# Kernel tuning notes

Hardware: AMD Instinct MI355X
Metric: run time of the kernel (lower is better)

The kernel has to match this reference:

```python
import jax, jax.numpy as jnp
import numpy as np

N = 100000
E = 3200000
IN_DIM, HID_DIM, OUT_DIM = 29, 64, 2


def setup_inputs() -> dict:
    key = jax.random.key(0)
    k1, k2, k3, k4, k5 = jax.random.split(key, 5)
    x = jax.random.normal(k1, (N, IN_DIM), dtype=jnp.float32)
    edge_index = jax.random.randint(k2, (2, E), 0, N, dtype=jnp.int64)
    # GCNConv params: glorot-ish weights, zero bias (bias added after aggregation)
    W1 = jax.random.normal(k3, (IN_DIM, HID_DIM), dtype=jnp.float32) * (1.0 / np.sqrt(IN_DIM))
    b1 = jnp.zeros((HID_DIM,), dtype=jnp.float32)
    W2 = jax.random.normal(k4, (HID_DIM, OUT_DIM), dtype=jnp.float32) * (1.0 / np.sqrt(HID_DIM))
    b2 = jnp.zeros((OUT_DIM,), dtype=jnp.float32)
    return {"x": x, "edge_index": edge_index, "W1": W1, "b1": b1, "W2": W2, "b2": b2}


def _gcn_norm(edge_index, n_nodes):
    # PyG gcn_norm with add_self_loops=True, symmetric D^-1/2 A D^-1/2
    loop = jnp.arange(n_nodes, dtype=edge_index.dtype)
    src = jnp.concatenate([edge_index[0], loop])
    dst = jnp.concatenate([edge_index[1], loop])
    deg = jax.ops.segment_sum(jnp.ones_like(dst, dtype=jnp.float32), dst, num_segments=n_nodes)
    dinv = jnp.where(deg > 0, jax.lax.rsqrt(deg), 0.0)
    norm = dinv[src] * dinv[dst]  # [E + N]
    return src, dst, norm


def _gcn_conv(x, src, dst, norm, W, b):
    h = x @ W                      # [N, d_out] -- transform first (smaller msgs)
    msg = h[src] * norm[:, None]   # [E+N, d_out] gather + scale
    out = jax.ops.segment_sum(msg, dst, num_segments=x.shape[0])  # scatter-add
    return out + b


def reference(x, edge_index, W1, b1, W2, b2):
    src, dst, norm = _gcn_norm(edge_index, x.shape[0])
    h = _gcn_conv(x, src, dst, norm, W1, b1)
    h = jax.nn.relu(h)
    out = _gcn_conv(h, src, dst, norm, W2, b2)
    return out
```

## Files before the change

kernel.cpp:

```cpp
#include <hip/hip_runtime.h>

#define N_NODES 100000
#define N_EDGES 3200000
#define IN_DIM  29
#define HID_DIM 64
#define NBUCK   1563
#define BNODES  64
#define CAP     2560
#define EPT     32
#define EPB     16384

#define OFF_CUR   0
#define OFF_DEGC  2048
#define OFF_DINV  102080
#define OFF_ROWS  202112
#define OFF_ROWE  302144
#define OFF_ZS    402176
#define OFF_EBUF  602240
#define OFF_XS    4603520

typedef unsigned uv2 __attribute__((ext_vector_type(2)));

static __device__ __forceinline__ unsigned short f2bf(float f) {
    unsigned u = __float_as_uint(f);
    u += 0x7fffu + ((u >> 16) & 1u);
    return (unsigned short)(u >> 16);
}

static __device__ __forceinline__ void unpack_add(float4& acc, uv2 a) {
    acc.x += __uint_as_float(a.x << 16);
    acc.y += __uint_as_float(a.x & 0xFFFF0000u);
    acc.z += __uint_as_float(a.y << 16);
    acc.w += __uint_as_float(a.y & 0xFFFF0000u);
}

__global__ __launch_bounds__(512) void partition_kernel(const int* __restrict__ ei,
        int* __restrict__ gcursor, int* __restrict__ ebuf) {
    __shared__ int lhist[NBUCK];
    __shared__ int lcur[NBUCK];
    int tid = threadIdx.x;
    for (int i = tid; i < NBUCK; i += 512) lhist[i] = 0;
    __syncthreads();

    int base = blockIdx.x * EPB + tid * EPT;
    int dv[EPT], sv[EPT];
    bool valid = (base < N_EDGES);
    if (valid) {
        const int4* dp = (const int4*)(ei + N_EDGES + base);
        const int4* sp = (const int4*)(ei + base);
        #pragma unroll
        for (int q = 0; q < 8; ++q) {
            int4 t = dp[q];
            dv[4*q+0] = t.x; dv[4*q+1] = t.y; dv[4*q+2] = t.z; dv[4*q+3] = t.w;
            int4 u = sp[q];
            sv[4*q+0] = u.x; sv[4*q+1] = u.y; sv[4*q+2] = u.z; sv[4*q+3] = u.w;
        }
        #pragma unroll
        for (int j = 0; j < EPT; ++j) atomicAdd(&lhist[dv[j] >> 6], 1);
    }
    __syncthreads();
    for (int i = tid; i < NBUCK; i += 512) {
        int c = lhist[i];
        lcur[i] = c ? (atomicAdd(&gcursor[i], c) + i * CAP) : 0;
    }
    __syncthreads();
    if (valid) {
        #pragma unroll
        for (int j = 0; j < EPT; ++j) {
            int d = dv[j];
            int pos = atomicAdd(&lcur[d >> 6], 1);
            ebuf[pos] = sv[j] | ((d & 63) << 17);
        }
    }
}

__global__ __launch_bounds__(256) void degcnt_kernel(const int* __restrict__ gcursor,
        const int* __restrict__ ebuf, const float* __restrict__ x,
        int* __restrict__ degc, float* __restrict__ dinv,
        unsigned int* __restrict__ xsb) {
    __shared__ int   cnt[BNODES];
    __shared__ float dls[BNODES];
    int b = blockIdx.x, tid = threadIdx.x;
    if (tid < BNODES) cnt[tid] = 0;
    __syncthreads();
    int base = b * CAP, sz = gcursor[b];
    for (int j = tid; j < sz; j += 256)
        atomicAdd(&cnt[((unsigned)ebuf[base + j]) >> 17], 1);
    __syncthreads();
    if (tid < BNODES) {
        int node = b * BNODES + tid;
        if (node < N_NODES) {
            int c = cnt[tid];
            degc[node] = c;
            float dn = rsqrtf((float)c + 1.0f);
            dinv[node] = dn;
            dls[tid] = dn;
        }
    }
    __syncthreads();
    for (int i = tid; i < BNODES * 16; i += 256) {
        int dl = i >> 4, kp = i & 15;
        int nd = b * BNODES + dl;
        if (nd < N_NODES) {
            float dn = dls[dl];
            int k0 = kp * 2, k1 = k0 + 1;
            float f0 = (k0 < IN_DIM) ? x[nd * IN_DIM + k0] * dn : 0.0f;
            float f1 = (k1 < IN_DIM) ? x[nd * IN_DIM + k1] * dn : 0.0f;
            xsb[(size_t)nd * 16 + kp] = (unsigned)f2bf(f0) | ((unsigned)f2bf(f1) << 16);
        }
    }
}

__global__ __launch_bounds__(256) void sortfused_kernel(const unsigned int* __restrict__ xs_,
        const int* __restrict__ gcursor, int* __restrict__ ebuf,
        const int* __restrict__ degc,
        int* __restrict__ rowStart, int* __restrict__ rowEnd,
        const float* __restrict__ W1, const float* __restrict__ b1,
        const float* __restrict__ W2, float* __restrict__ zs) {
    __shared__ float w1s[IN_DIM * HID_DIM];
    __shared__ float b1s[HID_DIM];
    __shared__ float w2s[HID_DIM * 2];
    __shared__ int   cnt[BNODES];
    __shared__ int   rs_l[BNODES];
    __shared__ int   cur[BNODES];
    __shared__ int   stage[CAP];
    int tid = threadIdx.x, b = blockIdx.x;
    for (int i = tid; i < IN_DIM * HID_DIM; i += 256) w1s[i] = W1[i];
    if (tid < HID_DIM) {
        b1s[tid] = b1[tid];
        w2s[tid * 2 + 0] = W2[tid * 2 + 0];
        w2s[tid * 2 + 1] = W2[tid * 2 + 1];
    }
    int base = b * CAP, sz = gcursor[b];
    if (tid < BNODES) {
        int node = b * BNODES + tid;
        cnt[tid] = (node < N_NODES) ? degc[node] : 0;
    }
    __syncthreads();

    if (tid < 64) {
        int c = cnt[tid];
        int incl = c;
        #pragma unroll
        for (int off = 1; off < 64; off <<= 1) {
            int t = __shfl_up(incl, off);
            if (tid >= off) incl += t;
        }
        int excl = incl - c;
        rs_l[tid] = excl;
        cur[tid]  = excl;
        int node = b * BNODES + tid;
        if (node < N_NODES) {
            rowStart[node] = base + excl;
            rowEnd[node]   = base + excl + c;
        }
    }
    __syncthreads();

    for (int j = tid; j < sz; j += 256) {
        unsigned p = (unsigned)ebuf[base + j];
        int pos = atomicAdd(&cur[p >> 17], 1);
        stage[pos] = p & 0x1FFFF;
    }
    __syncthreads();
    for (int j = tid; j < sz; j += 256)
        ebuf[base + j] = stage[j];

    int wave = tid >> 6, lane = tid & 63;
    int q = lane >> 3, m = lane & 7;
    const uv2* xsbv = (const uv2*)xs_;
    for (int dl = wave; dl < BNODES; dl += 4) {
        int node = b * BNODES + dl;
        if (node >= N_NODES) break;
        float4 acc = make_float4(0.f, 0.f, 0.f, 0.f);
        if (q == 0)
            unpack_add(acc, xsbv[(size_t)node * 8 + m]);
        int rs = rs_l[dl], re = rs + cnt[dl];
        int last = re - 1;
        for (int j = rs + q; j < re; j += 32) {
            int j1 = j + 8, j2 = j + 16, j3 = j + 24;
            int s0 = stage[j];
            int s1 = stage[min(j1, last)];
            int s2 = stage[min(j2, last)];
            int s3 = stage[min(j3, last)];
            uv2 a0 = xsbv[(size_t)s0 * 8 + m];
            uv2 a1 = xsbv[(size_t)s1 * 8 + m];
            uv2 a2 = xsbv[(size_t)s2 * 8 + m];
            uv2 a3 = xsbv[(size_t)s3 * 8 + m];
            unpack_add(acc, a0);
            if (j1 < re) unpack_add(acc, a1);
            if (j2 < re) unpack_add(acc, a2);
            if (j3 < re) unpack_add(acc, a3);
        }
        #pragma unroll
        for (int msk = 8; msk <= 32; msk <<= 1) {
            acc.x += __shfl_xor(acc.x, msk);
            acc.y += __shfl_xor(acc.y, msk);
            acc.z += __shfl_xor(acc.z, msk);
            acc.w += __shfl_xor(acc.w, msk);
        }
        float dn = rsqrtf((float)cnt[dl] + 1.0f);
        acc.x *= dn; acc.y *= dn; acc.z *= dn; acc.w *= dn;

        float h = b1s[lane];
        #pragma unroll
        for (int kk = 0; kk < IN_DIM; ++kk) {
            float comp = ((kk & 3) == 0) ? acc.x : ((kk & 3) == 1) ? acc.y
                       : ((kk & 3) == 2) ? acc.z : acc.w;
            h = fmaf(__shfl(comp, kk >> 2), w1s[kk * HID_DIM + lane], h);
        }
        h = fmaxf(h, 0.0f);

        float z0 = h * w2s[lane * 2 + 0];
        float z1 = h * w2s[lane * 2 + 1];
        #pragma unroll
        for (int off = 32; off > 0; off >>= 1) {
            z0 += __shfl_down(z0, off);
            z1 += __shfl_down(z1, off);
        }
        if (lane == 0) {
            zs[node * 2 + 0] = z0 * dn;
            zs[node * 2 + 1] = z1 * dn;
        }
    }
}

__global__ __launch_bounds__(256) void agg2_kernel(const float* __restrict__ zs,
        const int* __restrict__ rowStart, const int* __restrict__ rowEnd,
        const int* __restrict__ ebuf, const float* __restrict__ dinv,
        const float* __restrict__ b2, float* __restrict__ out) {
    int tid = threadIdx.x;
    int node = blockIdx.x * 16 + (tid >> 4);
    if (node >= N_NODES) return;
    int gl = tid & 15;
    const float2* zs2 = (const float2*)zs;
    float a0 = 0.0f, a1 = 0.0f, c0 = 0.0f, c1 = 0.0f;
    int rs = rowStart[node], re = rowEnd[node];
    int last = re - 1;
    for (int j = rs + gl; j < re; j += 32) {
        int j1 = j + 16;
        float2 za = zs2[ebuf[j]];
        float2 zb = zs2[ebuf[min(j1, last)]];
        a0 += za.x; a1 += za.y;
        if (j1 < re) { c0 += zb.x; c1 += zb.y; }
    }
    a0 += c0; a1 += c1;
    a0 += __shfl_xor(a0, 8); a1 += __shfl_xor(a1, 8);
    a0 += __shfl_xor(a0, 4); a1 += __shfl_xor(a1, 4);
    a0 += __shfl_xor(a0, 2); a1 += __shfl_xor(a1, 2);
    a0 += __shfl_xor(a0, 1); a1 += __shfl_xor(a1, 1);
    if (gl == 0) {
        float dn = dinv[node];
        float2 zself = zs2[node];
        float2 o;
        o.x = dn * (a0 + zself.x) + b2[0];
        o.y = dn * (a1 + zself.y) + b2[1];
        ((float2*)out)[node] = o;
    }
}

extern "C" void kernel_launch(void* const* d_in, const int* in_sizes, int n_in,
                              void* d_out, int out_size, void* d_ws, size_t ws_size,
                              hipStream_t stream) {
    const float* x  = (const float*)d_in[0];
    const int*   ei = (const int*)d_in[1];
    const float* W1 = (const float*)d_in[2];
    const float* b1 = (const float*)d_in[3];
    const float* W2 = (const float*)d_in[4];
    const float* b2 = (const float*)d_in[5];
    float* out = (float*)d_out;

    int*   wsi      = (int*)d_ws;
    float* wsf      = (float*)d_ws;
    int*   gcursor  = wsi + OFF_CUR;
    int*   degc     = wsi + OFF_DEGC;
    float* dinv     = wsf + OFF_DINV;
    int*   rowStart = wsi + OFF_ROWS;
    int*   rowEnd   = wsi + OFF_ROWE;
    float* zs       = wsf + OFF_ZS;
    int*   ebuf     = wsi + OFF_EBUF;
    unsigned int* xsb = (unsigned int*)(wsi + OFF_XS);

    hipMemsetAsync(gcursor, 0, NBUCK * sizeof(int), stream);
    partition_kernel<<<(N_EDGES + EPB - 1) / EPB, 512, 0, stream>>>(ei, gcursor, ebuf);
    degcnt_kernel<<<NBUCK, 256, 0, stream>>>(gcursor, ebuf, x, degc, dinv, xsb);
    sortfused_kernel<<<NBUCK, 256, 0, stream>>>(xsb, gcursor, ebuf, degc,
                                                rowStart, rowEnd, W1, b1, W2, zs);
    agg2_kernel<<<(N_NODES + 15) / 16, 256, 0, stream>>>(zs, rowStart, rowEnd, ebuf, dinv, b2, out);
}
```

Measured before the change: 237.9 us.

## Use coarser 256-node buckets with sub-block filtering and drop CSR writeback

Edges are now partitioned into 391 buckets of 256 destination nodes instead of 1563 buckets of 64. Each bucket is handled by 8 sub-blocks that each scan the whole bucket and keep only the edges for their own 32 nodes. This removes the sorted-ebuf writeback and the rowStart/rowEnd arrays. The second aggregation now accumulates into shared memory with atomics over the bucket, instead of walking per-node CSR rows. The cost is that every bucket is read 8 times in both the sort/fuse and aggregation kernels, and shared-memory float atomics replace register reductions.

```diff
diff --git a/kernel.cpp b/kernel.cpp
--- a/kernel.cpp
+++ b/kernel.cpp
@@ -4,20 +4,21 @@
 #define N_EDGES 3200000
 #define IN_DIM  29
 #define HID_DIM 64
-#define NBUCK   1563
-#define BNODES  64
-#define CAP     2560
-#define EPT     32
-#define EPB     16384
+#define NBUCK   391
+#define CNODES  256
+#define CAP     10240
+#define SUB     8
+#define SNODES  32
+#define CAP_S   1408
+#define EPT     8
+#define EPB     4096
 
 #define OFF_CUR   0
-#define OFF_DEGC  2048
-#define OFF_DINV  102080
-#define OFF_ROWS  202112
-#define OFF_ROWE  302144
-#define OFF_ZS    402176
-#define OFF_EBUF  602240
-#define OFF_XS    4603520
+#define OFF_DEGC  512
+#define OFF_DINV  100512
+#define OFF_ZS    200512
+#define OFF_EBUF  400512
+#define OFF_XS    4404352
 
 typedef unsigned uv2 __attribute__((ext_vector_type(2)));
 
@@ -49,14 +50,14 @@
         const int4* dp = (const int4*)(ei + N_EDGES + base);
         const int4* sp = (const int4*)(ei + base);
         #pragma unroll
-        for (int q = 0; q < 8; ++q) {
-            int4 t = dp[q];
-            dv[4*q+0] = t.x; dv[4*q+1] = t.y; dv[4*q+2] = t.z; dv[4*q+3] = t.w;
-            int4 u = sp[q];
-            sv[4*q+0] = u.x; sv[4*q+1] = u.y; sv[4*q+2] = u.z; sv[4*q+3] = u.w;
-        }
-        #pragma unroll
-        for (int j = 0; j < EPT; ++j) atomicAdd(&lhist[dv[j] >> 6], 1);
+        for (int qq = 0; qq < 2; ++qq) {
+            int4 t = dp[qq];
+            dv[4*qq+0] = t.x; dv[4*qq+1] = t.y; dv[4*qq+2] = t.z; dv[4*qq+3] = t.w;
+            int4 u = sp[qq];
+            sv[4*qq+0] = u.x; sv[4*qq+1] = u.y; sv[4*qq+2] = u.z; sv[4*qq+3] = u.w;
+        }
+        #pragma unroll
+        for (int j = 0; j < EPT; ++j) atomicAdd(&lhist[dv[j] >> 8], 1);
     }
     __syncthreads();
     for (int i = tid; i < NBUCK; i += 512) {
@@ -68,27 +69,27 @@
         #pragma unroll
         for (int j = 0; j < EPT; ++j) {
             int d = dv[j];
-            int pos = atomicAdd(&lcur[d >> 6], 1);
-            ebuf[pos] = sv[j] | ((d & 63) << 17);
-        }
-    }
-}
-
-__global__ __launch_bounds__(256) void degcnt_kernel(const int* __restrict__ gcursor,
+            int pos = atomicAdd(&lcur[d >> 8], 1);
+            ebuf[pos] = sv[j] | ((d & 255) << 17);
+        }
+    }
+}
+
+__global__ __launch_bounds__(1024) void degcnt_kernel(const int* __restrict__ gcursor,
         const int* __restrict__ ebuf, const float* __restrict__ x,
         int* __restrict__ degc, float* __restrict__ dinv,
         unsigned int* __restrict__ xsb) {
-    __shared__ int   cnt[BNODES];
-    __shared__ float dls[BNODES];
+    __shared__ int   cnt[CNODES];
+    __shared__ float dls[CNODES];
     int b = blockIdx.x, tid = threadIdx.x;
-    if (tid < BNODES) cnt[tid] = 0;
+    if (tid < CNODES) cnt[tid] = 0;
     __syncthreads();
     int base = b * CAP, sz = gcursor[b];
-    for (int j = tid; j < sz; j += 256)
+    for (int j = tid; j < sz; j += 1024)
         atomicAdd(&cnt[((unsigned)ebuf[base + j]) >> 17], 1);
     __syncthreads();
-    if (tid < BNODES) {
-        int node = b * BNODES + tid;
+    if (tid < CNODES) {
+        int node = b * CNODES + tid;
         if (node < N_NODES) {
             int c = cnt[tid];
             degc[node] = c;
@@ -98,9 +99,9 @@
         }
     }
     __syncthreads();
-    for (int i = tid; i < BNODES * 16; i += 256) {
+    for (int i = tid; i < CNODES * 16; i += 1024) {
         int dl = i >> 4, kp = i & 15;
-        int nd = b * BNODES + dl;
+        int nd = b * CNODES + dl;
         if (nd < N_NODES) {
             float dn = dls[dl];
             int k0 = kp * 2, k1 = k0 + 1;
@@ -112,72 +113,68 @@
 }
 
 __global__ __launch_bounds__(256) void sortfused_kernel(const unsigned int* __restrict__ xs_,
-        const int* __restrict__ gcursor, int* __restrict__ ebuf,
-        const int* __restrict__ degc,
-        int* __restrict__ rowStart, int* __restrict__ rowEnd,
+        const int* __restrict__ gcursor, const int* __restrict__ ebuf,
+        const int* __restrict__ degc, const float* __restrict__ dinv,
         const float* __restrict__ W1, const float* __restrict__ b1,
         const float* __restrict__ W2, float* __restrict__ zs) {
     __shared__ float w1s[IN_DIM * HID_DIM];
     __shared__ float b1s[HID_DIM];
     __shared__ float w2s[HID_DIM * 2];
-    __shared__ int   cnt[BNODES];
-    __shared__ int   rs_l[BNODES];
-    __shared__ int   cur[BNODES];
-    __shared__ int   stage[CAP];
-    int tid = threadIdx.x, b = blockIdx.x;
+    __shared__ int   cnt_s[SNODES];
+    __shared__ int   rs_s[SNODES];
+    __shared__ int   cur_s[SNODES];
+    __shared__ float dnv[SNODES];
+    __shared__ int   stage[CAP_S];
+    int tid = threadIdx.x;
+    int b = blockIdx.x >> 3, q = blockIdx.x & 7;
+    int nodeBase = b * CNODES + q * SNODES;
     for (int i = tid; i < IN_DIM * HID_DIM; i += 256) w1s[i] = W1[i];
     if (tid < HID_DIM) {
         b1s[tid] = b1[tid];
         w2s[tid * 2 + 0] = W2[tid * 2 + 0];
         w2s[tid * 2 + 1] = W2[tid * 2 + 1];
     }
-    int base = b * CAP, sz = gcursor[b];
-    if (tid < BNODES) {
-        int node = b * BNODES + tid;
-        cnt[tid] = (node < N_NODES) ? degc[node] : 0;
-    }
-    __syncthreads();
-
-    if (tid < 64) {
-        int c = cnt[tid];
+    if (tid < SNODES) {
+        int node = nodeBase + tid;
+        int c  = (node < N_NODES) ? degc[node] : 0;
+        dnv[tid] = (node < N_NODES) ? dinv[node] : 0.0f;
+        cnt_s[tid] = c;
         int incl = c;
         #pragma unroll
-        for (int off = 1; off < 64; off <<= 1) {
+        for (int off = 1; off < SNODES; off <<= 1) {
             int t = __shfl_up(incl, off);
             if (tid >= off) incl += t;
         }
         int excl = incl - c;
-        rs_l[tid] = excl;
-        cur[tid]  = excl;
-        int node = b * BNODES + tid;
-        if (node < N_NODES) {
-            rowStart[node] = base + excl;
-            rowEnd[node]   = base + excl + c;
-        }
-    }
-    __syncthreads();
-
+        rs_s[tid] = excl;
+        cur_s[tid] = excl;
+    }
+    __syncthreads();
+
+    int base = b * CAP, sz = gcursor[b];
     for (int j = tid; j < sz; j += 256) {
         unsigned p = (unsigned)ebuf[base + j];
-        int pos = atomicAdd(&cur[p >> 17], 1);
-        stage[pos] = p & 0x1FFFF;
-    }
-    __syncthreads();
-    for (int j = tid; j < sz; j += 256)
-        ebuf[base + j] = stage[j];
+        int dl8 = (int)(p >> 17);
+        if ((dl8 >> 5) == q) {
+            int pos = atomicAdd(&cur_s[dl8 & 31], 1);
+            stage[pos] = (int)(p & 0x1FFFF);
+        }
+    }
+    __syncthreads();
 
     int wave = tid >> 6, lane = tid & 63;
-    int q = lane >> 3, m = lane & 7;
+    int qs = lane >> 3, m = lane & 7;
     const uv2* xsbv = (const uv2*)xs_;
-    for (int dl = wave; dl < BNODES; dl += 4) {
-        int node = b * BNODES + dl;
+    for (int i = 0; i < 8; ++i) {
+        int dl = wave * 8 + i;
+        int node = nodeBase + dl;
         if (node >= N_NODES) break;
         float4 acc = make_float4(0.f, 0.f, 0.f, 0.f);
-        if (q == 0)
+        if (qs == 0)
             unpack_add(acc, xsbv[(size_t)node * 8 + m]);
-        int rs = rs_l[dl], re = rs + cnt[dl];
+        int rs = rs_s[dl], re = rs + cnt_s[dl];
         int last = re - 1;
-        for (int j = rs + q; j < re; j += 32) {
+        for (int j = rs + qs; j < re; j += 32) {
             int j1 = j + 8, j2 = j + 16, j3 = j + 24;
             int s0 = stage[j];
             int s1 = stage[min(j1, last)];
@@ -199,7 +196,7 @@
             acc.z += __shfl_xor(acc.z, msk);
             acc.w += __shfl_xor(acc.w, msk);
         }
-        float dn = rsqrtf((float)cnt[dl] + 1.0f);
+        float dn = dnv[dl];
         acc.x *= dn; acc.y *= dn; acc.z *= dn; acc.w *= dn;
 
         float h = b1s[lane];
@@ -226,36 +223,57 @@
 }
 
 __global__ __launch_bounds__(256) void agg2_kernel(const float* __restrict__ zs,
-        const int* __restrict__ rowStart, const int* __restrict__ rowEnd,
-        const int* __restrict__ ebuf, const float* __restrict__ dinv,
-        const float* __restrict__ b2, float* __restrict__ out) {
+        const int* __restrict__ gcursor, const int* __restrict__ ebuf,
+        const float* __restrict__ dinv, const float* __restrict__ b2,
+        float* __restrict__ out) {
+    __shared__ float aggz[SNODES * 2];
     int tid = threadIdx.x;
-    int node = blockIdx.x * 16 + (tid >> 4);
-    if (node >= N_NODES) return;
-    int gl = tid & 15;
+    int b = blockIdx.x >> 3, q = blockIdx.x & 7;
+    int nodeBase = b * CNODES + q * SNODES;
+    if (tid < SNODES * 2) {
+        int node = nodeBase + (tid >> 1);
+        aggz[tid] = (node < N_NODES) ? zs[node * 2 + (tid & 1)] : 0.0f;
+    }
+    __syncthreads();
     const float2* zs2 = (const float2*)zs;
-    float a0 = 0.0f, a1 = 0.0f, c0 = 0.0f, c1 = 0.0f;
-    int rs = rowStart[node], re = rowEnd[node];
-    int last = re - 1;
-    for (int j = rs + gl; j < re; j += 32) {
-        int j1 = j + 16;
-        float2 za = zs2[ebuf[j]];
-        float2 zb = zs2[ebuf[min(j1, last)]];
-        a0 += za.x; a1 += za.y;
-        if (j1 < re) { c0 += zb.x; c1 += zb.y; }
-    }
-    a0 += c0; a1 += c1;
-    a0 += __shfl_xor(a0, 8); a1 += __shfl_xor(a1, 8);
-    a0 += __shfl_xor(a0, 4); a1 += __shfl_xor(a1, 4);
-    a0 += __shfl_xor(a0, 2); a1 += __shfl_xor(a1, 2);
-    a0 += __shfl_xor(a0, 1); a1 += __shfl_xor(a1, 1);
-    if (gl == 0) {
-        float dn = dinv[node];
-        float2 zself = zs2[node];
-        float2 o;
-        o.x = dn * (a0 + zself.x) + b2[0];
-        o.y = dn * (a1 + zself.y) + b2[1];
-        ((float2*)out)[node] = o;
+    int base = b * CAP, sz = gcursor[b];
+    int last = sz - 1;
+    for (int j = tid; j < sz; j += 1024) {
+        int j1 = j + 256, j2 = j + 512, j3 = j + 768;
+        unsigned p0 = (unsigned)ebuf[base + j];
+        unsigned p1 = (unsigned)ebuf[base + min(j1, last)];
+        unsigned p2 = (unsigned)ebuf[base + min(j2, last)];
+        unsigned p3 = (unsigned)ebuf[base + min(j3, last)];
+        int d0 = (int)(p0 >> 17), d1 = (int)(p1 >> 17);
+        int d2 = (int)(p2 >> 17), d3 = (int)(p3 >> 17);
+        if ((d0 >> 5) == q) {
+            float2 zv = zs2[p0 & 0x1FFFF];
+            int o = (d0 & 31) * 2;
+            atomicAdd(&aggz[o], zv.x); atomicAdd(&aggz[o + 1], zv.y);
+        }
+        if (j1 < sz && (d1 >> 5) == q) {
+            float2 zv = zs2[p1 & 0x1FFFF];
+            int o = (d1 & 31) * 2;
+            atomicAdd(&aggz[o], zv.x); atomicAdd(&aggz[o + 1], zv.y);
+        }
+        if (j2 < sz && (d2 >> 5) == q) {
+            float2 zv = zs2[p2 & 0x1FFFF];
+            int o = (d2 & 31) * 2;
+            atomicAdd(&aggz[o], zv.x); atomicAdd(&aggz[o + 1], zv.y);
+        }
+        if (j3 < sz && (d3 >> 5) == q) {
+            float2 zv = zs2[p3 & 0x1FFFF];
+            int o = (d3 & 31) * 2;
+            atomicAdd(&aggz[o], zv.x); atomicAdd(&aggz[o + 1], zv.y);
+        }
+    }
+    __syncthreads();
+    if (tid < SNODES * 2) {
+        int node = nodeBase + (tid >> 1);
+        if (node < N_NODES) {
+            int c = tid & 1;
+            out[node * 2 + c] = dinv[node] * aggz[tid] + b2[c];
+        }
     }
 }
 
@@ -270,21 +288,19 @@
     const float* b2 = (const float*)d_in[5];
     float* out = (float*)d_out;
 
-    int*   wsi      = (int*)d_ws;
-    float* wsf      = (float*)d_ws;
-    int*   gcursor  = wsi + OFF_CUR;
-    int*   degc     = wsi + OFF_DEGC;
-    float* dinv     = wsf + OFF_DINV;
-    int*   rowStart = wsi + OFF_ROWS;
-    int*   rowEnd   = wsi + OFF_ROWE;
-    float* zs       = wsf + OFF_ZS;
-    int*   ebuf     = wsi + OFF_EBUF;
+    int*   wsi     = (int*)d_ws;
+    float* wsf     = (float*)d_ws;
+    int*   gcursor = wsi + OFF_CUR;
+    int*   degc    = wsi + OFF_DEGC;
+    float* dinv    = wsf + OFF_DINV;
+    float* zs      = wsf + OFF_ZS;
+    int*   ebuf    = wsi + OFF_EBUF;
     unsigned int* xsb = (unsigned int*)(wsi + OFF_XS);
 
     hipMemsetAsync(gcursor, 0, NBUCK * sizeof(int), stream);
     partition_kernel<<<(N_EDGES + EPB - 1) / EPB, 512, 0, stream>>>(ei, gcursor, ebuf);
-    degcnt_kernel<<<NBUCK, 256, 0, stream>>>(gcursor, ebuf, x, degc, dinv, xsb);
-    sortfused_kernel<<<NBUCK, 256, 0, stream>>>(xsb, gcursor, ebuf, degc,
-                                                rowStart, rowEnd, W1, b1, W2, zs);
-    agg2_kernel<<<(N_NODES + 15) / 16, 256, 0, stream>>>(zs, rowStart, rowEnd, ebuf, dinv, b2, out);
-}
+    degcnt_kernel<<<NBUCK, 1024, 0, stream>>>(gcursor, ebuf, x, degc, dinv, xsb);
+    sortfused_kernel<<<NBUCK * SUB, 256, 0, stream>>>(xsb, gcursor, ebuf, degc, dinv,
+                                                      W1, b1, W2, zs);
+    agg2_kernel<<<NBUCK * SUB, 256, 0, stream>>>(zs, gcursor, ebuf, dinv, b2, out);
+}
```

Result: slower. 262.4 us (+10.3%).
